# Performance work log

Hardware: AMD Instinct MI355X
Metric: run time of the kernel (lower is better)

## Reference

```python
import jax, jax.numpy as jnp
import numpy as np

HIDDEN = 4096
N_HEADS = 32
N_KV_HEADS = 8
D_HEAD = HIDDEN // N_HEADS  # 128
SEQ_LEN = 2048
ROPE_THETA = 10000.0


def _rope(t, start_index):
    # t: [L, n_heads, d_head]; rotate-half (Llama-style) RoPE
    L, _, d = t.shape
    inv_freq = 1.0 / (ROPE_THETA ** (jnp.arange(0, d, 2, dtype=jnp.float32) / d))  # [d/2]
    pos = jnp.arange(L, dtype=jnp.float32) + jnp.float32(start_index)  # [L]
    ang = pos[:, None] * inv_freq  # [L, d/2]
    cos = jnp.cos(ang)[:, None, :].astype(t.dtype)  # [L, 1, d/2]
    sin = jnp.sin(ang)[:, None, :].astype(t.dtype)
    t1, t2 = jnp.split(t, 2, axis=-1)
    return jnp.concatenate([t1 * cos - t2 * sin, t1 * sin + t2 * cos], axis=-1)


def setup_inputs() -> dict:
    key = jax.random.key(0)
    ks = jax.random.split(key, 5)
    s = 1.0 / np.sqrt(HIDDEN)
    return {
        "x": jax.random.normal(ks[0], (SEQ_LEN, HIDDEN), dtype=jnp.float32),
        "Wq": jax.random.normal(ks[1], (HIDDEN, N_HEADS * D_HEAD), dtype=jnp.float32) * s,
        "Wk": jax.random.normal(ks[2], (HIDDEN, N_KV_HEADS * D_HEAD), dtype=jnp.float32) * s,
        "Wv": jax.random.normal(ks[3], (HIDDEN, N_KV_HEADS * D_HEAD), dtype=jnp.float32) * s,
        "Wo": jax.random.normal(ks[4], (N_HEADS * D_HEAD, HIDDEN), dtype=jnp.float32) * s,
        "start_index": 0,
    }


def reference(x, Wq, Wk, Wv, Wo, start_index):
    # x: [L, hidden]; start_index==0 -> cache reset, so post-write cache == current k, v
    L, _ = x.shape
    q = (x @ Wq).reshape(L, N_HEADS, D_HEAD)
    k = (x @ Wk).reshape(L, N_KV_HEADS, D_HEAD)
    v = (x @ Wv).reshape(L, N_KV_HEADS, D_HEAD)
    q = _rope(q, start_index)
    k = _rope(k, start_index)
    # KV cache read: full cache is just [L] entries (prefill)
    S = L
    g = N_HEADS // N_KV_HEADS
    qh = q.transpose(1, 0, 2).reshape(N_KV_HEADS, g, L, D_HEAD)  # [kv, g, L, d]
    kh = k.transpose(1, 0, 2)  # [kv, S, d]
    vh = v.transpose(1, 0, 2)  # [kv, S, d]
    scale = 1.0 / np.sqrt(D_HEAD)
    scores = jnp.einsum('kgld,ksd->kgls', qh, kh) * jnp.asarray(scale, qh.dtype)
    # is_causal = (L > 1): tril(L, S) mask
    causal = jnp.tril(jnp.ones((L, S), dtype=bool))
    neg = jnp.asarray(jnp.finfo(scores.dtype).min, scores.dtype)
    scores = jnp.where(causal, scores, neg)
    attn = jax.nn.softmax(scores, axis=-1)
    out = jnp.einsum('kgls,ksd->kgld', attn, vh)  # [kv, g, L, d]
    out = out.reshape(N_HEADS, L, D_HEAD).transpose(1, 0, 2).reshape(L, N_HEADS * D_HEAD)
    return out @ Wo
```

## Files before the change

### kernel.cpp

```cpp
#include <hip/hip_runtime.h>

typedef unsigned short u16;
typedef float f32x4 __attribute__((ext_vector_type(4)));
typedef __bf16 bf16x8 __attribute__((ext_vector_type(8)));
typedef u16 u16x8 __attribute__((ext_vector_type(8)));

#define VMCNT(n) asm volatile("s_waitcnt vmcnt(" #n ")" ::: "memory")

static __device__ __forceinline__ u16 f2bf(float f) {
  union { float f; unsigned u; } v; v.f = f;
  unsigned r = v.u + 0x7fffu + ((v.u >> 16) & 1u);
  return (u16)(r >> 16);
}
static __device__ __forceinline__ u16 f2bf_n(float f) {
  __bf16 h = (__bf16)f;
  return __builtin_bit_cast(u16, h);
}
static __device__ __forceinline__ float bf2f(u16 x) {
  union { unsigned u; float f; } v; v.u = (unsigned)x << 16; return v.f;
}

static __device__ __forceinline__ f32x4 mfma16(u16x8 a, u16x8 b, f32x4 c) {
  return __builtin_amdgcn_mfma_f32_16x16x32_bf16(
      __builtin_bit_cast(bf16x8, a), __builtin_bit_cast(bf16x8, b), c, 0, 0, 0);
}

static __device__ __forceinline__ void load_lds16(const void* g, void* l) {
  __builtin_amdgcn_global_load_lds(
      (const __attribute__((address_space(1))) void*)g,
      (__attribute__((address_space(3))) void*)l, 16, 0, 0);
}

__global__ void cvt_f32_bf16_swz(const float* __restrict__ in, u16* __restrict__ out, int n8) {
  int i = blockIdx.x * blockDim.x + threadIdx.x;
  if (i >= n8) return;
  int row = i >> 9;
  int j = i & 511;
  int jp = (j & ~7) | ((j & 7) ^ (row & 7));
  const float* src = in + (size_t)i * 8;
  u16x8 o;
  #pragma unroll
  for (int e = 0; e < 8; e++) o[e] = f2bf(src[e]);
  *(u16x8*)(out + ((size_t)row << 12) + jp * 8) = o;
}

__global__ __launch_bounds__(256)
void transpose_cvt(const float* __restrict__ W, u16* __restrict__ Wt, int K, int N) {
  __shared__ float tile[128][33];
  const int k0 = blockIdx.x * 128, n0 = blockIdx.y * 32;
  const int tr = threadIdx.x >> 3;
  const int tc4 = (threadIdx.x & 7) * 4;
  #pragma unroll
  for (int it = 0; it < 4; it++) {
    int kl = it * 32 + tr;
    float4 v = *(const float4*)&W[(size_t)(k0 + kl) * N + n0 + tc4];
    tile[kl][tc4] = v.x; tile[kl][tc4 + 1] = v.y;
    tile[kl][tc4 + 2] = v.z; tile[kl][tc4 + 3] = v.w;
  }
  __syncthreads();
  const int nl = threadIdx.x >> 4;
  const int dch = threadIdx.x & 15;
  #pragma unroll
  for (int it = 0; it < 2; it++) {
    int n = n0 + it * 16 + nl;
    int sch = (dch & 8) | ((dch & 7) ^ (n & 7));
    u16x8 o;
    #pragma unroll
    for (int e = 0; e < 8; e++) o[e] = f2bf(tile[sch * 8 + e][it * 16 + nl]);
    *(u16x8*)&Wt[(size_t)n * K + k0 + dch * 8] = o;
  }
}

__global__ void rope_table_k(float2* __restrict__ tab, const int* __restrict__ start, int L) {
  int i = blockIdx.x * blockDim.x + threadIdx.x;
  if (i >= L * 64) return;
  int p = i >> 6, j = i & 63;
  float inv = powf(10000.0f, -(float)j / 64.0f);
  float ang = (float)(p + start[0]) * inv;
  tab[i] = make_float2(cosf(ang), sinf(ang));
}

__global__ void rope_apply_b(const u16* __restrict__ in, int istride, int icol,
                             u16* __restrict__ outp, const float2* __restrict__ tab,
                             int total, int H, float scale, int swz) {
  int i = blockIdx.x * blockDim.x + threadIdx.x;
  if (i >= total) return;
  int j8 = (i & 7) * 8;
  int h = (i >> 3) % H;
  int p = i / (8 * H);
  const u16* base = in + (size_t)p * istride + icol + h * 128;
  u16x8 a = *(const u16x8*)(base + j8);
  u16x8 b = *(const u16x8*)(base + j8 + 64);
  u16x8 o1, o2;
  #pragma unroll
  for (int e = 0; e < 8; e++) {
    float2 cs = tab[p * 64 + j8 + e];
    float av = bf2f(a[e]), bv = bf2f(b[e]);
    o1[e] = f2bf((av * cs.x - bv * cs.y) * scale);
    o2[e] = f2bf((av * cs.y + bv * cs.x) * scale);
  }
  int c1 = i & 7;
  int cs1 = swz ? (c1 ^ (p & 7)) : c1;
  u16* ob = outp + ((size_t)p * H + h) * 128 + cs1 * 8;
  *(u16x8*)ob = o1;
  *(u16x8*)(ob + 64) = o2;
}

template<int BN, bool OUT_BF16>
__global__ __launch_bounds__(256, 2)
void gemm8p(const u16* __restrict__ A, const u16* __restrict__ Bt,
            float* __restrict__ Cf, u16* __restrict__ Cb, int N, int K, int gm) {
  constexpr int N_REP = BN / 32;
  constexpr int NHALF = N_REP / 2;
  __shared__ alignas(16) u16 As[2][128 * 64];
  __shared__ alignas(16) u16 Bs[2][BN * 64];
  const int tid = threadIdx.x;
  const int lane = tid & 63;
  const int wid = tid >> 6;
  const int ql = lane & 15, kg = lane >> 4;
  const int wr = wid >> 1, wcn = wid & 1;

  const int nb = gridDim.x;
  const int b = blockIdx.x;
  const int swz = (b & 7) * (nb >> 3) + (b >> 3);
  const int m0 = (swz % gm) * 128;
  const int n0 = (swz / gm) * BN;

  const int srow = tid >> 3, schk = tid & 7;
  const u16* abase = A + (size_t)(m0 + srow) * K + schk * 8;
  const u16* bbase = Bt + (size_t)(n0 + srow) * K + schk * 8;

  auto stA = [&](int buf, int t, int c) {
    load_lds16(abase + (size_t)(c * 32) * K + t * 64,
               &As[buf][((c * 32 + srow) * 8 + schk) * 8]);
  };
  auto stB = [&](int buf, int t, int c) {
    load_lds16(bbase + (size_t)(c * 32) * K + t * 64,
               &Bs[buf][((c * 32 + srow) * 8 + schk) * 8]);
  };

  f32x4 acc[4][N_REP] = {};
  u16x8 af[2][2];
  u16x8 bfr[NHALF][2];
  u16x8 bpre[NHALF][2];
  const int NT = K / 64;

  stA(0, 0, 0); stA(0, 0, 1); stA(0, 0, 2); stA(0, 0, 3);
  #pragma unroll
  for (int c = 0; c < BN / 32; c++) stB(0, 0, c);
  VMCNT(0);
  __builtin_amdgcn_sched_barrier(0);
  __builtin_amdgcn_s_barrier();
  #pragma unroll
  for (int ni = 0; ni < NHALF; ni++)
    #pragma unroll
    for (int kk = 0; kk < 2; kk++) {
      int R = wcn * (16 * N_REP) + ni * 16 + ql;
      int ch = ((kk << 2) | kg) ^ (ql & 7);
      bpre[ni][kk] = *(const u16x8*)&Bs[0][(R * 8 + ch) * 8];
    }

  #pragma unroll 1
  for (int i = 0; i < NT / 2; i++) {
    const bool tail = (i == NT / 2 - 1);
    #pragma unroll
    for (int p = 0; p < 8; p++) {
      const int q = p & 3;
      const int m = q >> 1, n2 = q & 1;
      const int cbuf = (p < 4) ? 0 : 1;
      if (q == 0 || q == 2) {
        #pragma unroll
        for (int mi = 0; mi < 2; mi++)
          #pragma unroll
          for (int kk = 0; kk < 2; kk++) {
            int row = wr * 64 + m * 32 + mi * 16 + ql;
            int ch = ((kk << 2) | kg) ^ (ql & 7);
            af[mi][kk] = *(const u16x8*)&As[cbuf][(row * 8 + ch) * 8];
          }
      }
      if (q == 1) {
        #pragma unroll
        for (int ni = 0; ni < NHALF; ni++)
          #pragma unroll
          for (int kk = 0; kk < 2; kk++) {
            int R = wcn * (16 * N_REP) + 16 * NHALF + ni * 16 + ql;
            int ch = ((kk << 2) | kg) ^ (ql & 7);
            bfr[ni][kk] = *(const u16x8*)&Bs[cbuf][(R * 8 + ch) * 8];
          }
      }
      const int st = 2 * i + 1 + (p >= 4 ? 1 : 0);
      const int sbuf = st & 1;
      if (st < NT) {
        if constexpr (BN == 192) {
          if (q == 0) { stA(sbuf, st, 0); stA(sbuf, st, 2); stB(sbuf, st, 0); }
          else if (q == 1) { stB(sbuf, st, 1); stB(sbuf, st, 3); stB(sbuf, st, 4); }
          else if (q == 2) { stB(sbuf, st, 2); stB(sbuf, st, 5); }
          else { stA(sbuf, st, 1); stA(sbuf, st, 3); }
        } else {
          if (q == 0) { stA(sbuf, st, 0); stA(sbuf, st, 2); stB(sbuf, st, 0); }
          else if (q == 1) { stB(sbuf, st, 2); stB(sbuf, st, 1); }
          else if (q == 2) { stB(sbuf, st, 3); }
          else { stA(sbuf, st, 1); stA(sbuf, st, 3); }
        }
      }
      if (!tail || p < 4) {
        if constexpr (BN == 192) {
          if (q == 1) VMCNT(6);
          else if (q == 3) VMCNT(4);
          else VMCNT(5);
        } else {
          if (q == 0 || q == 1) VMCNT(5);
          else VMCNT(3);
        }
      } else {
        if (p == 4) VMCNT(2);
        else VMCNT(0);
      }
      __builtin_amdgcn_sched_barrier(0);
      __builtin_amdgcn_s_barrier();
      asm volatile("s_waitcnt lgkmcnt(0)" ::: "memory");
      __builtin_amdgcn_sched_barrier(0);
      if (q == 3) {
        const int nbuf = (p == 3) ? 1 : 0;
        const bool valid = (p == 3) || (2 * i + 2 < NT);
        if (valid) {
          #pragma unroll
          for (int ni = 0; ni < NHALF; ni++)
            #pragma unroll
            for (int kk = 0; kk < 2; kk++) {
              int R = wcn * (16 * N_REP) + ni * 16 + ql;
              int ch = ((kk << 2) | kg) ^ (ql & 7);
              bpre[ni][kk] = *(const u16x8*)&Bs[nbuf][(R * 8 + ch) * 8];
            }
        }
      }
      __builtin_amdgcn_s_setprio(1);
      #pragma unroll
      for (int mi = 0; mi < 2; mi++)
        #pragma unroll
        for (int ni = 0; ni < NHALF; ni++)
          #pragma unroll
          for (int kk = 0; kk < 2; kk++) {
            if (n2 == 0)
              acc[m * 2 + mi][ni] = mfma16(af[mi][kk], bpre[ni][kk], acc[m * 2 + mi][ni]);
            else
              acc[m * 2 + mi][NHALF + ni] = mfma16(af[mi][kk], bfr[ni][kk], acc[m * 2 + mi][NHALF + ni]);
          }
      __builtin_amdgcn_s_setprio(0);
      __builtin_amdgcn_sched_barrier(0);
      __builtin_amdgcn_s_barrier();
    }
  }

  #pragma unroll
  for (int a = 0; a < 4; a++) {
    #pragma unroll
    for (int j = 0; j < N_REP; j++) {
      int row0 = m0 + wr * 64 + (a >> 1) * 32 + (a & 1) * 16 + kg * 4;
      int col = n0 + wcn * (16 * N_REP) + j * 16 + ql;
      #pragma unroll
      for (int r = 0; r < 4; r++) {
        if constexpr (OUT_BF16)
          Cb[(size_t)(row0 + r) * N + col] = f2bf(acc[a][j][r]);
        else
          Cf[(size_t)(row0 + r) * N + col] = acc[a][j][r];
      }
    }
  }
}

__global__ __launch_bounds__(256, 2)
void attn_k(const u16* __restrict__ qkv, const u16* __restrict__ kr,
            const float2* __restrict__ tab, u16* __restrict__ out, float qscale) {
  __shared__ alignas(16) u16 Kls[2][64 * 128];
  __shared__ alignas(16) u16 Vt[2][128][72];
  __shared__ alignas(16) u16 Plds[4][16][72];
  const int tid = threadIdx.x;
  const int lane = tid & 63, wave = tid >> 6;
  const int ql = lane & 15, kg = lane >> 4;
  const int h = blockIdx.y, hk = h >> 2;

  const int sl4 = (tid & 15) * 4;
  const int d0s = (tid >> 4) * 8;
  const u16* vbase = qkv + 5120 + (size_t)hk * 128 + d0s;
  const int krow_s = tid >> 4, kcol_s = (tid & 15) * 8;
  const u16* kbase = kr + (size_t)hk * 128 + (size_t)krow_s * 1024 + kcol_s;

  int cur = 0;
  #pragma unroll 1
  for (int half_idx = 0; half_idx < 2; half_idx++) {
    const int tile = half_idx ? (31 - (int)blockIdx.x) : (int)blockIdx.x;
    const int q0 = tile * 64;
    const int qw = q0 + wave * 16;
    const int nsteps = tile + 1;

    u16x8 qf[4];
    {
      const u16* qsrc = qkv + (size_t)(qw + ql) * 6144 + h * 128;
      u16x8 qa[4];
      #pragma unroll
      for (int kk = 0; kk < 4; kk++)
        qa[kk] = *(const u16x8*)(qsrc + kk * 32 + kg * 8);
      const float2* trow = tab + (size_t)(qw + ql) * 64;
      #pragma unroll
      for (int pr = 0; pr < 2; pr++) {
        #pragma unroll
        for (int e = 0; e < 8; e++) {
          float2 cs = trow[pr * 32 + kg * 8 + e];
          float a = bf2f(qa[pr][e]);
          float b = bf2f(qa[pr + 2][e]);
          qf[pr][e]     = f2bf((a * cs.x - b * cs.y) * qscale);
          qf[pr + 2][e] = f2bf((a * cs.y + b * cs.x) * qscale);
        }
      }
    }

    f32x4 acc[8] = {};
    float m_run = -3e38f, l_run = 0.f;

    __syncthreads();
    cur = 0;
    u16x8 vreg[4];
    #pragma unroll
    for (int j = 0; j < 4; j++)
      vreg[j] = *(const u16x8*)(vbase + (size_t)(sl4 + j) * 6144);
    #pragma unroll
    for (int r = 0; r < 4; r++)
      load_lds16(kbase + (size_t)r * 16 * 1024, &Kls[0][(r * 256 + tid) * 8]);

    #pragma unroll 1
    for (int t = 0; t < nsteps; t++) {
      const int s0 = t * 64;
      const bool last = (t == nsteps - 1);
      #pragma unroll
      for (int e = 0; e < 8; e++) {
        ushort4 w;
        w.x = vreg[0][e]; w.y = vreg[1][e]; w.z = vreg[2][e]; w.w = vreg[3][e];
        *(ushort4*)&Vt[cur][d0s + e][sl4] = w;
      }
      __syncthreads();
      if (t + 1 < nsteps) {
        #pragma unroll
        for (int j = 0; j < 4; j++)
          vreg[j] = *(const u16x8*)(vbase + (size_t)(s0 + 64 + sl4 + j) * 6144);
        const u16* kn = kbase + (size_t)(s0 + 64) * 1024;
        #pragma unroll
        for (int r = 0; r < 4; r++)
          load_lds16(kn + (size_t)r * 16 * 1024, &Kls[cur ^ 1][(r * 256 + tid) * 8]);
      }
      f32x4 sc[4] = {};
      __builtin_amdgcn_s_setprio(1);
      #pragma unroll
      for (int sb = 0; sb < 4; sb++) {
        const u16* krow = &Kls[cur][(sb * 16 + ql) * 128];
        #pragma unroll
        for (int kk = 0; kk < 4; kk++) {
          u16x8 kf = *(const u16x8*)(krow + (((kk * 4 + kg) ^ (ql & 7)) * 8));
          sc[sb] = mfma16(kf, qf[kk], sc[sb]);
        }
      }
      __builtin_amdgcn_s_setprio(0);
      float mt;
      if (last) {
        const int qg = qw + ql;
        mt = -3e38f;
        #pragma unroll
        for (int sb = 0; sb < 4; sb++)
          #pragma unroll
          for (int r = 0; r < 4; r++) {
            int s = s0 + sb * 16 + kg * 4 + r;
            float v = (s > qg) ? -3e38f : sc[sb][r];
            sc[sb][r] = v;
            mt = fmaxf(mt, v);
          }
      } else {
        float a0 = fmaxf(sc[0][0], sc[0][1]), a1 = fmaxf(sc[0][2], sc[0][3]);
        float a2 = fmaxf(sc[1][0], sc[1][1]), a3 = fmaxf(sc[1][2], sc[1][3]);
        float a4 = fmaxf(sc[2][0], sc[2][1]), a5 = fmaxf(sc[2][2], sc[2][3]);
        float a6 = fmaxf(sc[3][0], sc[3][1]), a7 = fmaxf(sc[3][2], sc[3][3]);
        float b0 = fmaxf(a0, a1), b1 = fmaxf(a2, a3);
        float b2 = fmaxf(a4, a5), b3 = fmaxf(a6, a7);
        mt = fmaxf(fmaxf(b0, b1), fmaxf(b2, b3));
      }
      mt = fmaxf(mt, __shfl_xor(mt, 16, 64));
      mt = fmaxf(mt, __shfl_xor(mt, 32, 64));
      if (!__all(mt - m_run <= 11.5f)) {
        float m_new = fmaxf(m_run, mt);
        float fco = exp2f(m_run - m_new);
        float fr[4];
        #pragma unroll
        for (int r = 0; r < 4; r++) fr[r] = __shfl(fco, (lane & 48) | (kg * 4 + r), 64);
        #pragma unroll
        for (int db = 0; db < 8; db++)
          #pragma unroll
          for (int r = 0; r < 4; r++) acc[db][r] *= fr[r];
        l_run *= fco;
        m_run = m_new;
      }
      float rs = 0.f;
      #pragma unroll
      for (int sb = 0; sb < 4; sb++) {
        float e0 = exp2f(sc[sb][0] - m_run);
        float e1 = exp2f(sc[sb][1] - m_run);
        float e2 = exp2f(sc[sb][2] - m_run);
        float e3 = exp2f(sc[sb][3] - m_run);
        rs += (e0 + e1) + (e2 + e3);
        ushort4 pk;
        pk.x = f2bf_n(e0); pk.y = f2bf_n(e1);
        pk.z = f2bf_n(e2); pk.w = f2bf_n(e3);
        *(ushort4*)&Plds[wave][ql][sb * 16 + kg * 4] = pk;
      }
      rs += __shfl_xor(rs, 16, 64);
      rs += __shfl_xor(rs, 32, 64);
      l_run += rs;
      __builtin_amdgcn_s_setprio(1);
      #pragma unroll
      for (int hf = 0; hf < 2; hf++) {
        u16x8 pf = *(const u16x8*)&Plds[wave][ql][hf * 32 + kg * 8];
        #pragma unroll
        for (int db = 0; db < 8; db++) {
          u16x8 vf = *(const u16x8*)&Vt[cur][db * 16 + ql][hf * 32 + kg * 8];
          acc[db] = mfma16(pf, vf, acc[db]);
        }
      }
      __builtin_amdgcn_s_setprio(0);
      cur ^= 1;
    }

    float linv[4];
    #pragma unroll
    for (int r = 0; r < 4; r++)
      linv[r] = 1.f / __shfl(l_run, (lane & 48) | (kg * 4 + r), 64);
    #pragma unroll
    for (int db = 0; db < 8; db++) {
      int d = db * 16 + ql;
      #pragma unroll
      for (int r = 0; r < 4; r++) {
        int q = qw + kg * 4 + r;
        int col = (h * 128 + d) ^ ((q & 7) << 3);
        out[(size_t)q * 4096 + col] = f2bf_n(acc[db][r] * linv[r]);
      }
    }
  }
}

extern "C" void kernel_launch(void* const* d_in, const int* in_sizes, int n_in,
                              void* d_out, int out_size, void* d_ws, size_t ws_size,
                              hipStream_t stream) {
  const float* x  = (const float*)d_in[0];
  const float* Wq = (const float*)d_in[1];
  const float* Wk = (const float*)d_in[2];
  const float* Wv = (const float*)d_in[3];
  const float* Wo = (const float*)d_in[4];
  const int* start = (const int*)d_in[5];

  const int L = 2048, HID = 4096, NH = 32, NKV = 8;
  const int NQ = 4096, NKVD = 1024, NF = 6144;

  char* ws = (char*)d_ws;
  size_t off = 0;
  auto alloc = [&](size_t bytes) {
    void* p = ws + off;
    off += (bytes + 255) & ~(size_t)255;
    return p;
  };
  u16* x_b   = (u16*)alloc((size_t)L * HID * 2);
  u16* Wq_t  = (u16*)alloc((size_t)NQ * HID * 2);
  u16* Wk_t  = (u16*)alloc((size_t)NKVD * HID * 2);
  u16* Wv_t  = (u16*)alloc((size_t)NKVD * HID * 2);
  u16* Wo_t  = (u16*)alloc((size_t)HID * NQ * 2);
  u16* k_r   = (u16*)alloc((size_t)L * NKVD * 2);
  float2* tab = (float2*)alloc((size_t)L * 64 * sizeof(float2));
  u16* qkv_b  = (u16*)d_out;
  u16* attn_b = Wq_t;

  const float qscale = 0.08838834764831845f * 1.4426950408889634f;

  cvt_f32_bf16_swz<<<(L * HID / 8 + 255) / 256, 256, 0, stream>>>(x, x_b, L * HID / 8);
  transpose_cvt<<<dim3(HID / 128, NQ / 32), 256, 0, stream>>>(Wq, Wq_t, HID, NQ);
  transpose_cvt<<<dim3(HID / 128, NKVD / 32), 256, 0, stream>>>(Wk, Wk_t, HID, NKVD);
  transpose_cvt<<<dim3(HID / 128, NKVD / 32), 256, 0, stream>>>(Wv, Wv_t, HID, NKVD);
  transpose_cvt<<<dim3(NQ / 128, HID / 32), 256, 0, stream>>>(Wo, Wo_t, NQ, HID);
  rope_table_k<<<(L * 64 + 255) / 256, 256, 0, stream>>>(tab, start, L);

  gemm8p<192, true><<<512, 256, 0, stream>>>(x_b, Wq_t, nullptr, qkv_b, NF, HID, 16);

  rope_apply_b<<<(L * NKV * 8 + 255) / 256, 256, 0, stream>>>(qkv_b, NF, NQ, k_r, tab, L * NKV * 8, NKV, 1.0f, 1);

  attn_k<<<dim3(16, NH), 256, 0, stream>>>(qkv_b, k_r, tab, attn_b, qscale);

  gemm8p<128, false><<<512, 256, 0, stream>>>(attn_b, Wo_t, (float*)d_out, nullptr, HID, NQ, 16);
}
```

Baseline: 322.9 us.

## Process two query heads per attention block to share K/V tiles

Each attention block now handles two query heads of the same GQA group for one query tile, so every K and V tile loaded into LDS feeds twice as many MFMAs. It also drops the old pairing of a light and a heavy causal tile per block in favour of a 1D grid of 512 blocks that launches the long tiles first. V now uses a single LDS buffer with an extra barrier at the end of each step. This roughly doubles the accumulator and Q-fragment registers, which may cut occupancy under launch_bounds(256,2), and puts the load balance in the hands of the hardware scheduler.

```diff
diff --git a/kernel.cpp b/kernel.cpp
--- a/kernel.cpp
+++ b/kernel.cpp
@@ -273,93 +273,94 @@
 void attn_k(const u16* __restrict__ qkv, const u16* __restrict__ kr,
             const float2* __restrict__ tab, u16* __restrict__ out, float qscale) {
   __shared__ alignas(16) u16 Kls[2][64 * 128];
-  __shared__ alignas(16) u16 Vt[2][128][72];
-  __shared__ alignas(16) u16 Plds[4][16][72];
+  __shared__ alignas(16) u16 Vt[128][72];
+  __shared__ alignas(16) u16 Plds[4][16][152];
   const int tid = threadIdx.x;
   const int lane = tid & 63, wave = tid >> 6;
   const int ql = lane & 15, kg = lane >> 4;
-  const int h = blockIdx.y, hk = h >> 2;
+
+  const int bx = blockIdx.x;
+  const int tile = (bx < 256) ? (31 - (bx >> 4)) : ((bx - 256) >> 4);
+  const int hp = bx & 15;
+  const int h0 = hp * 2, hk = hp >> 1;
+  const int q0 = tile * 64;
+  const int qw = q0 + wave * 16;
+  const int nsteps = tile + 1;
 
   const int sl4 = (tid & 15) * 4;
   const int d0s = (tid >> 4) * 8;
   const u16* vbase = qkv + 5120 + (size_t)hk * 128 + d0s;
-  const int krow_s = tid >> 4, kcol_s = (tid & 15) * 8;
-  const u16* kbase = kr + (size_t)hk * 128 + (size_t)krow_s * 1024 + kcol_s;
+  const u16* kbase = kr + (size_t)hk * 128 + (size_t)(tid >> 4) * 1024 + (tid & 15) * 8;
+
+  u16x8 qf[2][4];
+  #pragma unroll
+  for (int h2 = 0; h2 < 2; h2++) {
+    const u16* qsrc = qkv + (size_t)(qw + ql) * 6144 + (h0 + h2) * 128;
+    u16x8 qa[4];
+    #pragma unroll
+    for (int kk = 0; kk < 4; kk++)
+      qa[kk] = *(const u16x8*)(qsrc + kk * 32 + kg * 8);
+    const float2* trow = tab + (size_t)(qw + ql) * 64;
+    #pragma unroll
+    for (int pr = 0; pr < 2; pr++) {
+      #pragma unroll
+      for (int e = 0; e < 8; e++) {
+        float2 cs = trow[pr * 32 + kg * 8 + e];
+        float a = bf2f(qa[pr][e]);
+        float b = bf2f(qa[pr + 2][e]);
+        qf[h2][pr][e]     = f2bf((a * cs.x - b * cs.y) * qscale);
+        qf[h2][pr + 2][e] = f2bf((a * cs.y + b * cs.x) * qscale);
+      }
+    }
+  }
+
+  f32x4 acc[2][8] = {};
+  float m_run[2] = {-3e38f, -3e38f}, l_run[2] = {0.f, 0.f};
+
+  u16x8 vreg[4];
+  #pragma unroll
+  for (int j = 0; j < 4; j++)
+    vreg[j] = *(const u16x8*)(vbase + (size_t)(sl4 + j) * 6144);
+  #pragma unroll
+  for (int r = 0; r < 4; r++)
+    load_lds16(kbase + (size_t)r * 16 * 1024, &Kls[0][(r * 256 + tid) * 8]);
 
   int cur = 0;
   #pragma unroll 1
-  for (int half_idx = 0; half_idx < 2; half_idx++) {
-    const int tile = half_idx ? (31 - (int)blockIdx.x) : (int)blockIdx.x;
-    const int q0 = tile * 64;
-    const int qw = q0 + wave * 16;
-    const int nsteps = tile + 1;
-
-    u16x8 qf[4];
-    {
-      const u16* qsrc = qkv + (size_t)(qw + ql) * 6144 + h * 128;
-      u16x8 qa[4];
-      #pragma unroll
-      for (int kk = 0; kk < 4; kk++)
-        qa[kk] = *(const u16x8*)(qsrc + kk * 32 + kg * 8);
-      const float2* trow = tab + (size_t)(qw + ql) * 64;
-      #pragma unroll
-      for (int pr = 0; pr < 2; pr++) {
-        #pragma unroll
-        for (int e = 0; e < 8; e++) {
-          float2 cs = trow[pr * 32 + kg * 8 + e];
-          float a = bf2f(qa[pr][e]);
-          float b = bf2f(qa[pr + 2][e]);
-          qf[pr][e]     = f2bf((a * cs.x - b * cs.y) * qscale);
-          qf[pr + 2][e] = f2bf((a * cs.y + b * cs.x) * qscale);
-        }
-      }
-    }
-
-    f32x4 acc[8] = {};
-    float m_run = -3e38f, l_run = 0.f;
-
+  for (int t = 0; t < nsteps; t++) {
+    const int s0 = t * 64;
+    const bool last = (t == nsteps - 1);
+    #pragma unroll
+    for (int e = 0; e < 8; e++) {
+      ushort4 w;
+      w.x = vreg[0][e]; w.y = vreg[1][e]; w.z = vreg[2][e]; w.w = vreg[3][e];
+      *(ushort4*)&Vt[d0s + e][sl4] = w;
+    }
     __syncthreads();
-    cur = 0;
-    u16x8 vreg[4];
-    #pragma unroll
-    for (int j = 0; j < 4; j++)
-      vreg[j] = *(const u16x8*)(vbase + (size_t)(sl4 + j) * 6144);
-    #pragma unroll
-    for (int r = 0; r < 4; r++)
-      load_lds16(kbase + (size_t)r * 16 * 1024, &Kls[0][(r * 256 + tid) * 8]);
-
-    #pragma unroll 1
-    for (int t = 0; t < nsteps; t++) {
-      const int s0 = t * 64;
-      const bool last = (t == nsteps - 1);
-      #pragma unroll
-      for (int e = 0; e < 8; e++) {
-        ushort4 w;
-        w.x = vreg[0][e]; w.y = vreg[1][e]; w.z = vreg[2][e]; w.w = vreg[3][e];
-        *(ushort4*)&Vt[cur][d0s + e][sl4] = w;
-      }
-      __syncthreads();
-      if (t + 1 < nsteps) {
-        #pragma unroll
-        for (int j = 0; j < 4; j++)
-          vreg[j] = *(const u16x8*)(vbase + (size_t)(s0 + 64 + sl4 + j) * 6144);
-        const u16* kn = kbase + (size_t)(s0 + 64) * 1024;
-        #pragma unroll
-        for (int r = 0; r < 4; r++)
-          load_lds16(kn + (size_t)r * 16 * 1024, &Kls[cur ^ 1][(r * 256 + tid) * 8]);
-      }
-      f32x4 sc[4] = {};
-      __builtin_amdgcn_s_setprio(1);
-      #pragma unroll
-      for (int sb = 0; sb < 4; sb++) {
-        const u16* krow = &Kls[cur][(sb * 16 + ql) * 128];
-        #pragma unroll
-        for (int kk = 0; kk < 4; kk++) {
-          u16x8 kf = *(const u16x8*)(krow + (((kk * 4 + kg) ^ (ql & 7)) * 8));
-          sc[sb] = mfma16(kf, qf[kk], sc[sb]);
-        }
-      }
-      __builtin_amdgcn_s_setprio(0);
+    if (t + 1 < nsteps) {
+      #pragma unroll
+      for (int j = 0; j < 4; j++)
+        vreg[j] = *(const u16x8*)(vbase + (size_t)(s0 + 64 + sl4 + j) * 6144);
+      const u16* kn = kbase + (size_t)(s0 + 64) * 1024;
+      #pragma unroll
+      for (int r = 0; r < 4; r++)
+        load_lds16(kn + (size_t)r * 16 * 1024, &Kls[cur ^ 1][(r * 256 + tid) * 8]);
+    }
+    f32x4 sc[2][4] = {};
+    __builtin_amdgcn_s_setprio(1);
+    #pragma unroll
+    for (int sb = 0; sb < 4; sb++) {
+      const u16* krow = &Kls[cur][(sb * 16 + ql) * 128];
+      #pragma unroll
+      for (int kk = 0; kk < 4; kk++) {
+        u16x8 kf = *(const u16x8*)(krow + (((kk * 4 + kg) ^ (ql & 7)) * 8));
+        sc[0][sb] = mfma16(kf, qf[0][kk], sc[0][sb]);
+        sc[1][sb] = mfma16(kf, qf[1][kk], sc[1][sb]);
+      }
+    }
+    __builtin_amdgcn_s_setprio(0);
+    #pragma unroll
+    for (int h2 = 0; h2 < 2; h2++) {
       float mt;
       if (last) {
         const int qg = qw + ql;
@@ -369,76 +370,81 @@
           #pragma unroll
           for (int r = 0; r < 4; r++) {
             int s = s0 + sb * 16 + kg * 4 + r;
-            float v = (s > qg) ? -3e38f : sc[sb][r];
-            sc[sb][r] = v;
+            float v = (s > qg) ? -3e38f : sc[h2][sb][r];
+            sc[h2][sb][r] = v;
             mt = fmaxf(mt, v);
           }
       } else {
-        float a0 = fmaxf(sc[0][0], sc[0][1]), a1 = fmaxf(sc[0][2], sc[0][3]);
-        float a2 = fmaxf(sc[1][0], sc[1][1]), a3 = fmaxf(sc[1][2], sc[1][3]);
-        float a4 = fmaxf(sc[2][0], sc[2][1]), a5 = fmaxf(sc[2][2], sc[2][3]);
-        float a6 = fmaxf(sc[3][0], sc[3][1]), a7 = fmaxf(sc[3][2], sc[3][3]);
-        float b0 = fmaxf(a0, a1), b1 = fmaxf(a2, a3);
-        float b2 = fmaxf(a4, a5), b3 = fmaxf(a6, a7);
-        mt = fmaxf(fmaxf(b0, b1), fmaxf(b2, b3));
+        float a0 = fmaxf(sc[h2][0][0], sc[h2][0][1]), a1 = fmaxf(sc[h2][0][2], sc[h2][0][3]);
+        float a2 = fmaxf(sc[h2][1][0], sc[h2][1][1]), a3 = fmaxf(sc[h2][1][2], sc[h2][1][3]);
+        float a4 = fmaxf(sc[h2][2][0], sc[h2][2][1]), a5 = fmaxf(sc[h2][2][2], sc[h2][2][3]);
+        float a6 = fmaxf(sc[h2][3][0], sc[h2][3][1]), a7 = fmaxf(sc[h2][3][2], sc[h2][3][3]);
+        mt = fmaxf(fmaxf(fmaxf(a0, a1), fmaxf(a2, a3)),
+                   fmaxf(fmaxf(a4, a5), fmaxf(a6, a7)));
       }
       mt = fmaxf(mt, __shfl_xor(mt, 16, 64));
       mt = fmaxf(mt, __shfl_xor(mt, 32, 64));
-      if (!__all(mt - m_run <= 11.5f)) {
-        float m_new = fmaxf(m_run, mt);
-        float fco = exp2f(m_run - m_new);
+      if (!__all(mt - m_run[h2] <= 11.5f)) {
+        float m_new = fmaxf(m_run[h2], mt);
+        float fco = exp2f(m_run[h2] - m_new);
         float fr[4];
         #pragma unroll
         for (int r = 0; r < 4; r++) fr[r] = __shfl(fco, (lane & 48) | (kg * 4 + r), 64);
         #pragma unroll
         for (int db = 0; db < 8; db++)
           #pragma unroll
-          for (int r = 0; r < 4; r++) acc[db][r] *= fr[r];
-        l_run *= fco;
-        m_run = m_new;
+          for (int r = 0; r < 4; r++) acc[h2][db][r] *= fr[r];
+        l_run[h2] *= fco;
+        m_run[h2] = m_new;
       }
       float rs = 0.f;
       #pragma unroll
       for (int sb = 0; sb < 4; sb++) {
-        float e0 = exp2f(sc[sb][0] - m_run);
-        float e1 = exp2f(sc[sb][1] - m_run);
-        float e2 = exp2f(sc[sb][2] - m_run);
-        float e3 = exp2f(sc[sb][3] - m_run);
+        float e0 = exp2f(sc[h2][sb][0] - m_run[h2]);
+        float e1 = exp2f(sc[h2][sb][1] - m_run[h2]);
+        float e2 = exp2f(sc[h2][sb][2] - m_run[h2]);
+        float e3 = exp2f(sc[h2][sb][3] - m_run[h2]);
         rs += (e0 + e1) + (e2 + e3);
         ushort4 pk;
         pk.x = f2bf_n(e0); pk.y = f2bf_n(e1);
         pk.z = f2bf_n(e2); pk.w = f2bf_n(e3);
-        *(ushort4*)&Plds[wave][ql][sb * 16 + kg * 4] = pk;
+        *(ushort4*)&Plds[wave][ql][h2 * 80 + sb * 16 + kg * 4] = pk;
       }
       rs += __shfl_xor(rs, 16, 64);
       rs += __shfl_xor(rs, 32, 64);
-      l_run += rs;
-      __builtin_amdgcn_s_setprio(1);
-      #pragma unroll
-      for (int hf = 0; hf < 2; hf++) {
-        u16x8 pf = *(const u16x8*)&Plds[wave][ql][hf * 32 + kg * 8];
-        #pragma unroll
-        for (int db = 0; db < 8; db++) {
-          u16x8 vf = *(const u16x8*)&Vt[cur][db * 16 + ql][hf * 32 + kg * 8];
-          acc[db] = mfma16(pf, vf, acc[db]);
-        }
-      }
-      __builtin_amdgcn_s_setprio(0);
-      cur ^= 1;
-    }
-
+      l_run[h2] += rs;
+    }
+    __builtin_amdgcn_s_setprio(1);
+    #pragma unroll
+    for (int hf = 0; hf < 2; hf++) {
+      u16x8 pf0 = *(const u16x8*)&Plds[wave][ql][hf * 32 + kg * 8];
+      u16x8 pf1 = *(const u16x8*)&Plds[wave][ql][80 + hf * 32 + kg * 8];
+      #pragma unroll
+      for (int db = 0; db < 8; db++) {
+        u16x8 vf = *(const u16x8*)&Vt[db * 16 + ql][hf * 32 + kg * 8];
+        acc[0][db] = mfma16(pf0, vf, acc[0][db]);
+        acc[1][db] = mfma16(pf1, vf, acc[1][db]);
+      }
+    }
+    __builtin_amdgcn_s_setprio(0);
+    __syncthreads();
+    cur ^= 1;
+  }
+
+  #pragma unroll
+  for (int h2 = 0; h2 < 2; h2++) {
     float linv[4];
     #pragma unroll
     for (int r = 0; r < 4; r++)
-      linv[r] = 1.f / __shfl(l_run, (lane & 48) | (kg * 4 + r), 64);
+      linv[r] = 1.f / __shfl(l_run[h2], (lane & 48) | (kg * 4 + r), 64);
     #pragma unroll
     for (int db = 0; db < 8; db++) {
       int d = db * 16 + ql;
       #pragma unroll
       for (int r = 0; r < 4; r++) {
         int q = qw + kg * 4 + r;
-        int col = (h * 128 + d) ^ ((q & 7) << 3);
-        out[(size_t)q * 4096 + col] = f2bf_n(acc[db][r] * linv[r]);
+        int col = ((h0 + h2) * 128 + d) ^ ((q & 7) << 3);
+        out[(size_t)q * 4096 + col] = f2bf_n(acc[h2][db][r] * linv[r]);
       }
     }
   }
@@ -487,7 +493,7 @@
 
   rope_apply_b<<<(L * NKV * 8 + 255) / 256, 256, 0, stream>>>(qkv_b, NF, NQ, k_r, tab, L * NKV * 8, NKV, 1.0f, 1);
 
-  attn_k<<<dim3(16, NH), 256, 0, stream>>>(qkv_b, k_r, tab, attn_b, qscale);
+  attn_k<<<512, 256, 0, stream>>>(qkv_b, k_r, tab, attn_b, qscale);
 
   gemm8p<128, false><<<512, 256, 0, stream>>>(attn_b, Wo_t, (float*)d_out, nullptr, HID, NQ, 16);
 }
```

Result: slower. 333.8 us (+3.4%).

## Pre-transpose V into swizzled global layout and stream it via direct-to-LDS loads

Applied to the files above, without the earlier changes.

Adds a separate kernel that transposes V from the fused QKV buffer into a per-KV-head [d][s] layout with an XOR swizzle. The attention kernel then loads V tiles straight into LDS with the same async load path used for K, instead of loading rows into registers and transposing them into LDS each step. This removes per-step register-to-LDS transpose writes and frees registers. The cost is an extra kernel launch and an extra global round trip for V.

```diff
diff --git a/kernel.cpp b/kernel.cpp
--- a/kernel.cpp
+++ b/kernel.cpp
@@ -68,6 +68,28 @@
     #pragma unroll
     for (int e = 0; e < 8; e++) o[e] = f2bf(tile[sch * 8 + e][it * 16 + nl]);
     *(u16x8*)&Wt[(size_t)n * K + k0 + dch * 8] = o;
+  }
+}
+
+__global__ __launch_bounds__(256)
+void vtrans_k(const u16* __restrict__ qkv, u16* __restrict__ vt) {
+  __shared__ u16 tile[32][33];
+  int tx = threadIdx.x & 31, ty = threadIdx.x >> 5;
+  int s0 = blockIdx.x * 32;
+  int d0 = (blockIdx.y & 3) * 32;
+  int hk = blockIdx.y >> 2;
+  const u16* src = qkv + 5120 + (size_t)hk * 128;
+  #pragma unroll
+  for (int i = ty; i < 32; i += 8)
+    tile[i][tx] = src[(size_t)(s0 + i) * 6144 + d0 + tx];
+  __syncthreads();
+  u16* dst = vt + (size_t)hk * 128 * 2048;
+  #pragma unroll
+  for (int i = ty; i < 32; i += 8) {
+    int d = d0 + i;
+    int s = s0 + tx;
+    int sw = (s & ~63) | ((((s >> 3) & 7) ^ (d & 7)) << 3) | (s & 7);
+    dst[(size_t)d * 2048 + sw] = tile[tx][i];
   }
 }
 
@@ -271,20 +293,18 @@
 
 __global__ __launch_bounds__(256, 2)
 void attn_k(const u16* __restrict__ qkv, const u16* __restrict__ kr,
-            const float2* __restrict__ tab, u16* __restrict__ out, float qscale) {
+            const u16* __restrict__ vt, const float2* __restrict__ tab,
+            u16* __restrict__ out, float qscale) {
   __shared__ alignas(16) u16 Kls[2][64 * 128];
-  __shared__ alignas(16) u16 Vt[2][128][72];
+  __shared__ alignas(16) u16 Vls[2][128 * 64];
   __shared__ alignas(16) u16 Plds[4][16][72];
   const int tid = threadIdx.x;
   const int lane = tid & 63, wave = tid >> 6;
   const int ql = lane & 15, kg = lane >> 4;
   const int h = blockIdx.y, hk = h >> 2;
 
-  const int sl4 = (tid & 15) * 4;
-  const int d0s = (tid >> 4) * 8;
-  const u16* vbase = qkv + 5120 + (size_t)hk * 128 + d0s;
-  const int krow_s = tid >> 4, kcol_s = (tid & 15) * 8;
-  const u16* kbase = kr + (size_t)hk * 128 + (size_t)krow_s * 1024 + kcol_s;
+  const u16* kbase = kr + (size_t)hk * 128 + (size_t)(tid >> 4) * 1024 + (tid & 15) * 8;
+  const u16* vbase = vt + (size_t)hk * 128 * 2048 + (size_t)(tid >> 3) * 2048 + (tid & 7) * 8;
 
   int cur = 0;
   #pragma unroll 1
@@ -320,33 +340,27 @@
 
     __syncthreads();
     cur = 0;
-    u16x8 vreg[4];
-    #pragma unroll
-    for (int j = 0; j < 4; j++)
-      vreg[j] = *(const u16x8*)(vbase + (size_t)(sl4 + j) * 6144);
     #pragma unroll
     for (int r = 0; r < 4; r++)
       load_lds16(kbase + (size_t)r * 16 * 1024, &Kls[0][(r * 256 + tid) * 8]);
+    #pragma unroll
+    for (int r = 0; r < 4; r++)
+      load_lds16(vbase + (size_t)r * 32 * 2048, &Vls[0][(r * 256 + tid) * 8]);
 
     #pragma unroll 1
     for (int t = 0; t < nsteps; t++) {
       const int s0 = t * 64;
       const bool last = (t == nsteps - 1);
-      #pragma unroll
-      for (int e = 0; e < 8; e++) {
-        ushort4 w;
-        w.x = vreg[0][e]; w.y = vreg[1][e]; w.z = vreg[2][e]; w.w = vreg[3][e];
-        *(ushort4*)&Vt[cur][d0s + e][sl4] = w;
-      }
       __syncthreads();
       if (t + 1 < nsteps) {
-        #pragma unroll
-        for (int j = 0; j < 4; j++)
-          vreg[j] = *(const u16x8*)(vbase + (size_t)(s0 + 64 + sl4 + j) * 6144);
         const u16* kn = kbase + (size_t)(s0 + 64) * 1024;
         #pragma unroll
         for (int r = 0; r < 4; r++)
           load_lds16(kn + (size_t)r * 16 * 1024, &Kls[cur ^ 1][(r * 256 + tid) * 8]);
+        const u16* vn = vbase + (s0 + 64);
+        #pragma unroll
+        for (int r = 0; r < 4; r++)
+          load_lds16(vn + (size_t)r * 32 * 2048, &Vls[cur ^ 1][(r * 256 + tid) * 8]);
       }
       f32x4 sc[4] = {};
       __builtin_amdgcn_s_setprio(1);
@@ -419,7 +433,8 @@
         u16x8 pf = *(const u16x8*)&Plds[wave][ql][hf * 32 + kg * 8];
         #pragma unroll
         for (int db = 0; db < 8; db++) {
-          u16x8 vf = *(const u16x8*)&Vt[cur][db * 16 + ql][hf * 32 + kg * 8];
+          u16x8 vf = *(const u16x8*)&Vls[cur][((db * 16 + ql) << 6) +
+                                              (((hf * 4 + kg) ^ (ql & 7)) << 3)];
           acc[db] = mfma16(pf, vf, acc[db]);
         }
       }
@@ -470,6 +485,7 @@
   u16* Wv_t  = (u16*)alloc((size_t)NKVD * HID * 2);
   u16* Wo_t  = (u16*)alloc((size_t)HID * NQ * 2);
   u16* k_r   = (u16*)alloc((size_t)L * NKVD * 2);
+  u16* vt_b  = (u16*)alloc((size_t)NKV * 128 * L * 2);
   float2* tab = (float2*)alloc((size_t)L * 64 * sizeof(float2));
   u16* qkv_b  = (u16*)d_out;
   u16* attn_b = Wq_t;
@@ -486,8 +502,9 @@
   gemm8p<192, true><<<512, 256, 0, stream>>>(x_b, Wq_t, nullptr, qkv_b, NF, HID, 16);
 
   rope_apply_b<<<(L * NKV * 8 + 255) / 256, 256, 0, stream>>>(qkv_b, NF, NQ, k_r, tab, L * NKV * 8, NKV, 1.0f, 1);
-
-  attn_k<<<dim3(16, NH), 256, 0, stream>>>(qkv_b, k_r, tab, attn_b, qscale);
+  vtrans_k<<<dim3(L / 32, 32), 256, 0, stream>>>(qkv_b, vt_b);
+
+  attn_k<<<dim3(16, NH), 256, 0, stream>>>(qkv_b, k_r, vt_b, tab, attn_b, qscale);
 
   gemm8p<128, false><<<512, 256, 0, stream>>>(attn_b, Wo_t, (float*)d_out, nullptr, HID, NQ, 16);
 }
```

After: 315.6 us. -2.3%, faster.
